# Performance work log

Measured on AMD Instinct MI355X. Metric: run time of the kernel, lower is better.

The kernel has to match this reference:

```python
import jax, jax.numpy as jnp
import numpy as np

D_MODEL = 512
N_HEADS = 8
D_K = D_MODEL // N_HEADS  # 64
MAX_LEN = 5000


def _positional_encoding(d_model, max_len):
    pe = np.zeros((max_len, d_model), dtype=np.float32)
    position = np.arange(max_len, dtype=np.float32)[:, None]
    div_term = np.exp(np.arange(0, d_model, 2, dtype=np.float32) * (-np.log(10000.0) / d_model))
    pe[:, 0::2] = np.sin(position * div_term)
    pe[:, 1::2] = np.cos(position * div_term)
    return jnp.asarray(pe)


def _layer_norm(x, gamma, beta, eps):
    mu = jnp.mean(x, axis=-1, keepdims=True)
    var = jnp.mean(jnp.square(x - mu), axis=-1, keepdims=True)
    return (x - mu) * jax.lax.rsqrt(var + eps) * gamma + beta


def setup_inputs() -> dict:
    key = jax.random.key(0)
    ks = jax.random.split(key, 5)
    s = 1.0 / np.sqrt(D_MODEL)
    return {
        "x": jax.random.normal(ks[0], (4, 2048, D_MODEL), dtype=jnp.float32),
        "ln1_g": jnp.ones((D_MODEL,), jnp.float32),
        "ln1_b": jnp.zeros((D_MODEL,), jnp.float32),
        "wq": jax.random.normal(ks[1], (D_MODEL, D_MODEL), jnp.float32) * s,
        "wk": jax.random.normal(ks[2], (D_MODEL, D_MODEL), jnp.float32) * s,
        "wv": jax.random.normal(ks[3], (D_MODEL, D_MODEL), jnp.float32) * s,
        "wfc": jax.random.normal(ks[4], (D_MODEL, D_MODEL), jnp.float32) * s,
        "ln2_g": jnp.ones((D_MODEL,), jnp.float32),
        "ln2_b": jnp.zeros((D_MODEL,), jnp.float32),
    }


def reference(x, ln1_g, ln1_b, wq, wk, wv, wfc, ln2_g, ln2_b):
    B, T, D = x.shape
    residual0 = x
    # outer pre-norm (nn.LayerNorm default eps=1e-5)
    h = _layer_norm(x, ln1_g, ln1_b, 1e-5)
    # sinusoidal positional encoding
    h = h + _positional_encoding(D_MODEL, MAX_LEN)[:T]
    residual1 = h
    # projections -> [B, H, T, d]
    q = (h @ wq).reshape(B, T, N_HEADS, D_K).transpose(0, 2, 1, 3)
    k = (h @ wk).reshape(B, T, N_HEADS, D_K).transpose(0, 2, 1, 3)
    v = (h @ wv).reshape(B, T, N_HEADS, D_K).transpose(0, 2, 1, 3)
    scale = 1.0 / np.sqrt(D_K).astype(np.float32)
    attn = jnp.einsum("bhqd,bhkd->bhqk", q * scale, k)
    causal = jnp.tril(jnp.ones((T, T), dtype=bool))  # subsequent mask
    attn = jnp.where(causal, attn, jnp.float32(-1e9))
    attn = jax.nn.softmax(attn, axis=-1)
    o = jnp.einsum("bhqk,bhkd->bhqd", attn, v)
    o = o.transpose(0, 2, 1, 3).reshape(B, T, D)
    o = o @ wfc
    # inner post-attention residual + LayerNorm (eps=1e-6)
    h2 = _layer_norm(o + residual1, ln2_g, ln2_b, 1e-6)
    return h2 + residual0
```

## Files before the change

kernel.cpp:

```cpp
#include <hip/hip_runtime.h>
#include <hip/hip_bf16.h>

#define B_ 4
#define T_ 2048
#define D_ 512

typedef __attribute__((ext_vector_type(8))) short short8;
typedef __attribute__((ext_vector_type(4))) short short4v;
typedef __attribute__((ext_vector_type(4))) float float4v;
typedef unsigned short bf16_t;

__device__ __forceinline__ bf16_t f2bf(float f) {
  unsigned int u = __builtin_bit_cast(unsigned int, f);
  unsigned int r = (u + 0x7fffu + ((u >> 16) & 1u)) >> 16;
  return (bf16_t)r;
}
__device__ __forceinline__ float bf2f(bf16_t b) {
  unsigned int u = ((unsigned int)b) << 16;
  return __builtin_bit_cast(float, u);
}

__device__ __forceinline__ float fast_exp2(float x) {
#if __has_builtin(__builtin_amdgcn_exp2f)
  return __builtin_amdgcn_exp2f(x);
#else
  float r;
  asm("v_exp_f32 %0, %1" : "=v"(r) : "v"(x));
  return r;
#endif
}

__device__ __forceinline__ unsigned cvt_pk_bf16(float lo, float hi) {
  unsigned r;
  asm("v_cvt_pk_bf16_f32 %0, %1, %2" : "=v"(r) : "v"(lo), "v"(hi));
  return r;
}

__device__ __forceinline__ float waveReduceSum(float v) {
#pragma unroll
  for (int m = 32; m >= 1; m >>= 1) v += __shfl_xor(v, m, 64);
  return v;
}

__device__ __forceinline__ void gld16(const bf16_t* g, bf16_t* l) {
  __builtin_amdgcn_global_load_lds(
      (const __attribute__((address_space(1))) void*)g,
      (__attribute__((address_space(3))) void*)l, 16, 0, 0);
}

__global__ __launch_bounds__(256) void pre_kernel(
    const float* __restrict__ x, const float* __restrict__ g,
    const float* __restrict__ bb,
    const float* __restrict__ wq, const float* __restrict__ wk,
    const float* __restrict__ wv, const float* __restrict__ wfc,
    bf16_t* __restrict__ h_bf16,
    bf16_t* __restrict__ wqkvT, bf16_t* __restrict__ wfcT) {
  if (blockIdx.x >= 2048) {
    int bid = blockIdx.x - 2048;
#pragma unroll 4
    for (int i = 0; i < 16; ++i) {
      int idx = bid * 4096 + i * 256 + threadIdx.x;
      if (idx < 786432) {
        int n = idx >> 9, k = idx & 511;
        const float* src = (n < 512) ? wq : ((n < 1024) ? wk : wv);
        float scl = (n < 512) ? 1.4426950408889634f
                              : ((n < 1024) ? 0.125f : 1.0f);
        int c = n & 511;
        wqkvT[idx] = f2bf(src[k * 512 + c] * scl);
      } else {
        int j = idx - 786432;
        int n = j >> 9, k = j & 511;
        wfcT[j] = f2bf(wfc[k * 512 + n]);
      }
    }
    return;
  }
  int wave = threadIdx.x >> 6, lane = threadIdx.x & 63;
  int row = blockIdx.x * 4 + wave;
  int pos = row & (T_ - 1);
  const float* xr = x + (size_t)row * D_;
  int c0 = lane * 8;
  float v[8];
  float4 a = *(const float4*)(xr + c0);
  float4 b4 = *(const float4*)(xr + c0 + 4);
  v[0]=a.x; v[1]=a.y; v[2]=a.z; v[3]=a.w;
  v[4]=b4.x; v[5]=b4.y; v[6]=b4.z; v[7]=b4.w;
  float s = 0.f;
#pragma unroll
  for (int j = 0; j < 8; ++j) s += v[j];
  s = waveReduceSum(s);
  float mu = s * (1.f / 512.f);
  float q = 0.f;
#pragma unroll
  for (int j = 0; j < 8; ++j) { float d = v[j] - mu; q += d * d; }
  q = waveReduceSum(q);
  float rstd = rsqrtf(q * (1.f / 512.f) + 1e-5f);
  bf16_t* hb = h_bf16 + (size_t)row * D_;
  float fpos = (float)pos;
#pragma unroll
  for (int jp = 0; jp < 4; ++jp) {
    int col = c0 + jp * 2;
    float dt = fast_exp2((float)col * (-13.287712379549449f / 512.0f));
    float ang = fpos * dt;
    float hn0 = (v[2 * jp] - mu) * rstd * g[col] + bb[col] + __sinf(ang);
    float hn1 = (v[2 * jp + 1] - mu) * rstd * g[col + 1] + bb[col + 1] + __cosf(ang);
    hb[col] = f2bf(hn0);
    hb[col + 1] = f2bf(hn1);
  }
}

template <typename EPI>
__device__ __forceinline__ void gemm_body(const bf16_t* __restrict__ A,
                                          const bf16_t* __restrict__ Bt,
                                          int m0, int n0, bf16_t* As, bf16_t* Bs,
                                          EPI epi) {
  const int tid = threadIdx.x;
  const int w = tid >> 6, lane = tid & 63;
  const int ln = lane & 15, quad = lane >> 4;
  const int wy = w >> 1, wx = w & 1;
  const int sw = ln & 7;

  float4v acc[4][4];
  float4v z = {0.f, 0.f, 0.f, 0.f};
#pragma unroll
  for (int i = 0; i < 4; ++i)
#pragma unroll
    for (int j = 0; j < 4; ++j) acc[i][j] = z;

  for (int k0 = 0; k0 < 512; k0 += 64) {
#pragma unroll
    for (int i = 0; i < 4; ++i) {
      int cbase = w * 256 + i * 64;
      int chunk = cbase + lane;
      int row = chunk >> 3;
      int lb = (chunk & 7) ^ (row & 7);
      gld16(A + (size_t)(m0 + row) * 512 + k0 + lb * 8, As + cbase * 8);
      gld16(Bt + (size_t)(n0 + row) * 512 + k0 + lb * 8, Bs + cbase * 8);
    }
    __syncthreads();
#pragma unroll
    for (int c = 0; c < 2; ++c) {
      short8 af[4], bf[4];
#pragma unroll
      for (int mt = 0; mt < 4; ++mt)
        af[mt] = *(const short8*)(As + (wy * 64 + mt * 16 + ln) * 64 + (((c * 4 + quad) ^ sw)) * 8);
#pragma unroll
      for (int nt = 0; nt < 4; ++nt)
        bf[nt] = *(const short8*)(Bs + (wx * 64 + nt * 16 + ln) * 64 + (((c * 4 + quad) ^ sw)) * 8);
#pragma unroll
      for (int mt = 0; mt < 4; ++mt)
#pragma unroll
        for (int nt = 0; nt < 4; ++nt)
          acc[mt][nt] = __builtin_amdgcn_mfma_f32_16x16x32_bf16(af[mt], bf[nt], acc[mt][nt], 0, 0, 0);
    }
    __syncthreads();
  }
#pragma unroll
  for (int mt = 0; mt < 4; ++mt)
#pragma unroll
    for (int r = 0; r < 4; ++r) {
      int row = m0 + wy * 64 + mt * 16 + quad * 4 + r;
#pragma unroll
      for (int nt = 0; nt < 4; ++nt) {
        int col = n0 + wx * 64 + nt * 16 + ln;
        epi(row, col, acc[mt][nt][r]);
      }
    }
}

__global__ __launch_bounds__(256) void gemm_qkvt_kernel(
    const bf16_t* __restrict__ h_bf, const bf16_t* __restrict__ wqkvT,
    bf16_t* __restrict__ qk, bf16_t* __restrict__ vT) {
  __shared__ __align__(16) bf16_t As[128 * 64];
  __shared__ __align__(16) bf16_t Bs[128 * 64];
  int bx = blockIdx.x;
  if (bx < 512) {
    int m0 = (bx >> 3) * 128, n0 = (bx & 7) * 128;
    gemm_body(h_bf, wqkvT, m0, n0, As, Bs,
              [&](int row, int col, float v) { qk[(size_t)row * 1024 + col] = f2bf(v); });
  } else {
    int local = bx - 512;
    int m0 = (local >> 6) * 128, n0 = (local & 63) * 128;
    gemm_body(wqkvT + 1024 * 512, h_bf, m0, n0, As, Bs,
              [&](int row, int col, float v) { vT[(size_t)row * 8192 + col] = f2bf(v); });
  }
}

__global__ __launch_bounds__(256) void gemm_out_kernel(
    const bf16_t* __restrict__ attn, const bf16_t* __restrict__ wfcT,
    const bf16_t* __restrict__ h_bf, bf16_t* __restrict__ o2r) {
  __shared__ __align__(16) bf16_t As[128 * 64];
  __shared__ __align__(16) bf16_t Bs[128 * 64];
  int bx = blockIdx.x;
  int m0 = (bx >> 2) * 128, n0 = (bx & 3) * 128;
  gemm_body(attn, wfcT, m0, n0, As, Bs, [&](int row, int col, float v) {
    size_t o = (size_t)row * 512 + col;
    o2r[o] = f2bf(v + bf2f(h_bf[o]));
  });
}

__global__ __launch_bounds__(256) void attn_kernel(const bf16_t* __restrict__ qk,
                                                   const bf16_t* __restrict__ vT,
                                                   bf16_t* __restrict__ out) {
  __shared__ __align__(16) bf16_t Ks[2][64 * 64];
  __shared__ __align__(16) bf16_t Vs[2][64 * 64];
  const int bx = blockIdx.x;
  const int qt = 31 - (bx >> 5);
  const int bh = bx & 31;
  const int b = bh >> 3, h = bh & 7;
  const int tid = threadIdx.x;
  const int w = tid >> 6, lane = tid & 63;
  const int ln = lane & 15, quad = lane >> 4;
  const int sw = ln & 7;

  short8 qf0, qf1;
  {
    size_t qrow = ((size_t)b * T_ + qt * 64 + w * 16 + ln) * 1024 + h * 64;
    qf0 = *(const short8*)(qk + qrow + quad * 8);
    qf1 = *(const short8*)(qk + qrow + 32 + quad * 8);
  }
  float4v z = {0.f, 0.f, 0.f, 0.f};
  float4v oacc[4];
#pragma unroll
  for (int i = 0; i < 4; ++i) oacc[i] = z;
  float m_s = -1e30f, l_s = 0.f;

  const bf16_t* kbase = qk + (size_t)b * T_ * 1024 + 512 + h * 64;
  const bf16_t* vbase = vT + (size_t)(h * 64) * 8192 + (size_t)b * T_;

  const int cb0 = w * 128, cb1 = w * 128 + 64;
  const int ch0 = cb0 + lane, ch1 = cb1 + lane;
  const int r0 = ch0 >> 3, r1 = ch1 >> 3;
  const int lb0 = (ch0 & 7) ^ (r0 & 7), lb1 = (ch1 & 7) ^ (r1 & 7);
  const bf16_t* kg0 = kbase + (size_t)r0 * 1024 + lb0 * 8;
  const bf16_t* kg1 = kbase + (size_t)r1 * 1024 + lb1 * 8;
  const bf16_t* vg0 = vbase + (size_t)r0 * 8192 + lb0 * 8;
  const bf16_t* vg1 = vbase + (size_t)r1 * 8192 + lb1 * 8;

  auto stage2 = [&](int buf) {
    gld16(kg0, Ks[buf] + cb0 * 8);
    gld16(kg1, Ks[buf] + cb1 * 8);
    gld16(vg0, Vs[buf] + cb0 * 8);
    gld16(vg1, Vs[buf] + cb1 * 8);
    kg0 += 64 * 1024; kg1 += 64 * 1024;
    vg0 += 64;        vg1 += 64;
  };

  auto compute = [&](const bf16_t* Kc, const bf16_t* Vc, bool mask) {
    float sv[4][4];
#pragma unroll
    for (int mt = 0; mt < 4; ++mt) {
      float4v st = z;
      int row = mt * 16 + ln;
      short8 a0 = *(const short8*)(Kc + row * 64 + ((0 + quad) ^ sw) * 8);
      short8 a1 = *(const short8*)(Kc + row * 64 + ((4 + quad) ^ sw) * 8);
      st = __builtin_amdgcn_mfma_f32_16x16x32_bf16(a0, qf0, st, 0, 0, 0);
      st = __builtin_amdgcn_mfma_f32_16x16x32_bf16(a1, qf1, st, 0, 0, 0);
#pragma unroll
      for (int r = 0; r < 4; ++r) {
        float v = st[r];
        if (mask) {
          int kloc = mt * 16 + quad * 4 + r;
          if (kloc > w * 16 + ln) v = -1e30f;
        }
        sv[mt][r] = v;
      }
    }
    float mx = sv[0][0];
#pragma unroll
    for (int mt = 0; mt < 4; ++mt)
#pragma unroll
      for (int r = 0; r < 4; ++r) mx = fmaxf(mx, sv[mt][r]);
    mx = fmaxf(mx, __shfl_xor(mx, 16, 64));
    mx = fmaxf(mx, __shfl_xor(mx, 32, 64));
    if (!__all(mx <= m_s + 8.0f)) {
      float mn = fmaxf(m_s, mx);
      float alpha = fast_exp2(m_s - mn);
      m_s = mn;
      l_s *= alpha;
#pragma unroll
      for (int dt = 0; dt < 4; ++dt)
#pragma unroll
        for (int r = 0; r < 4; ++r) oacc[dt][r] *= alpha;
    }
    float rs = 0.f;
#pragma unroll
    for (int mt = 0; mt < 4; ++mt)
#pragma unroll
      for (int r = 0; r < 4; ++r) {
        float p = fast_exp2(sv[mt][r] - m_s);
        sv[mt][r] = p;
        rs += p;
      }
    rs += __shfl_xor(rs, 16, 64);
    rs += __shfl_xor(rs, 32, 64);
    l_s += rs;
    short4v pf[4];
#pragma unroll
    for (int mt = 0; mt < 4; ++mt) {
      uint2 pp;
      pp.x = cvt_pk_bf16(sv[mt][0], sv[mt][1]);
      pp.y = cvt_pk_bf16(sv[mt][2], sv[mt][3]);
      pf[mt] = __builtin_bit_cast(short4v, pp);
    }
#pragma unroll
    for (int dt = 0; dt < 4; ++dt) {
      int row = dt * 16 + ln;
#pragma unroll
      for (int mt = 0; mt < 4; ++mt) {
        short4v av = *(const short4v*)(Vc + row * 64 + ((2 * mt + (quad >> 1)) ^ sw) * 8 + (quad & 1) * 4);
        oacc[dt] = __builtin_amdgcn_mfma_f32_16x16x16bf16_1k(av, pf[mt], oacc[dt], 0, 0, 0);
      }
    }
  };

  stage2(0);
  __syncthreads();
  for (int kt = 0; kt < qt; ++kt) {
    int cur = kt & 1;
    stage2(cur ^ 1);
    compute(Ks[cur], Vs[cur], false);
    __syncthreads();
  }
  compute(Ks[qt & 1], Vs[qt & 1], true);

  float inv = 1.0f / l_s;
  size_t obase = ((size_t)b * T_ + qt * 64 + w * 16 + ln) * 512 + h * 64;
#pragma unroll
  for (int dt = 0; dt < 4; ++dt) {
    short4v o4;
#pragma unroll
    for (int r = 0; r < 4; ++r) o4[r] = (short)f2bf(oacc[dt][r] * inv);
    *(short4v*)(out + obase + dt * 16 + quad * 4) = o4;
  }
}

__global__ __launch_bounds__(256) void ln2_kernel(
    const bf16_t* __restrict__ o2r, const float* __restrict__ x,
    const float* __restrict__ g, const float* __restrict__ bb,
    float* __restrict__ out) {
  int wave = threadIdx.x >> 6, lane = threadIdx.x & 63;
  int row = blockIdx.x * 4 + wave;
  size_t ro = (size_t)row * D_;
  int c0 = lane * 8;
  short8 ov = *(const short8*)(o2r + ro + c0);
  float t[8];
#pragma unroll
  for (int j = 0; j < 8; ++j) t[j] = bf2f((bf16_t)ov[j]);
  float s = 0.f;
#pragma unroll
  for (int j = 0; j < 8; ++j) s += t[j];
  s = waveReduceSum(s);
  float mu = s * (1.f / 512.f);
  float q = 0.f;
#pragma unroll
  for (int j = 0; j < 8; ++j) { float d = t[j] - mu; q += d * d; }
  q = waveReduceSum(q);
  float rstd = rsqrtf(q * (1.f / 512.f) + 1e-6f);
  float4 x0 = *(const float4*)(x + ro + c0);
  float4 x1 = *(const float4*)(x + ro + c0 + 4);
  float xr[8] = {x0.x, x0.y, x0.z, x0.w, x1.x, x1.y, x1.z, x1.w};
  float o[8];
#pragma unroll
  for (int j = 0; j < 8; ++j) {
    int col = c0 + j;
    o[j] = (t[j] - mu) * rstd * g[col] + bb[col] + xr[j];
  }
  float4 w0 = {o[0], o[1], o[2], o[3]};
  float4 w1 = {o[4], o[5], o[6], o[7]};
  *(float4*)(out + ro + c0) = w0;
  *(float4*)(out + ro + c0 + 4) = w1;
}

extern "C" void kernel_launch(void* const* d_in, const int* in_sizes, int n_in,
                              void* d_out, int out_size, void* d_ws, size_t ws_size,
                              hipStream_t stream) {
  const float* x   = (const float*)d_in[0];
  const float* g1  = (const float*)d_in[1];
  const float* b1  = (const float*)d_in[2];
  const float* wq  = (const float*)d_in[3];
  const float* wk  = (const float*)d_in[4];
  const float* wv  = (const float*)d_in[5];
  const float* wfc = (const float*)d_in[6];
  const float* g2  = (const float*)d_in[7];
  const float* b2  = (const float*)d_in[8];
  float* out = (float*)d_out;

  char* ws = (char*)d_ws;
  const size_t O_HBF  = 0;
  const size_t O_WQKV = 8388608;
  const size_t O_WFC  = 9961472;
  const size_t O_QK   = 10485760;
  const size_t O_VT   = 27262976;
  const size_t O_ATTN = 35651584;
  const size_t O_O2R  = 44040192;
  const size_t WS_NEED = 52428800;
  if (ws_size < WS_NEED) return;

  bf16_t* h_bf  = (bf16_t*)(ws + O_HBF);
  bf16_t* wqkvT = (bf16_t*)(ws + O_WQKV);
  bf16_t* wfcT  = (bf16_t*)(ws + O_WFC);
  bf16_t* qk    = (bf16_t*)(ws + O_QK);
  bf16_t* vT    = (bf16_t*)(ws + O_VT);
  bf16_t* attn  = (bf16_t*)(ws + O_ATTN);
  bf16_t* o2r   = (bf16_t*)(ws + O_O2R);

  pre_kernel<<<dim3(2304), dim3(256), 0, stream>>>(x, g1, b1, wq, wk, wv, wfc,
                                                   h_bf, wqkvT, wfcT);
  gemm_qkvt_kernel<<<dim3(768), dim3(256), 0, stream>>>(h_bf, wqkvT, qk, vT);
  attn_kernel<<<dim3(1024), dim3(256), 0, stream>>>(qk, vT, attn);
  gemm_out_kernel<<<dim3(256), dim3(256), 0, stream>>>(attn, wfcT, h_bf, o2r);
  ln2_kernel<<<dim3(2048), dim3(256), 0, stream>>>(o2r, x, g2, b2, out);
}
```

Measured before the change: 180.7 us.

## Split causal attention KV range across two blocks and merge with combine kernel

Each query tile's key range is split into two halves handled by separate blocks, doubling the attention grid. Each half writes an unnormalized partial output plus its per-row max and sum. A new combine kernel rescales and merges the two partials into the final attention output. This aims to improve load balance and occupancy across the causal triangle, at the cost of an extra kernel launch and additional memory traffic for the partials and stats. The max and sum reductions were also reshaped into shallower trees.

```diff
diff --git a/kernel.cpp b/kernel.cpp
--- a/kernel.cpp
+++ b/kernel.cpp
@@ -201,18 +201,26 @@
 
 __global__ __launch_bounds__(256) void attn_kernel(const bf16_t* __restrict__ qk,
                                                    const bf16_t* __restrict__ vT,
-                                                   bf16_t* __restrict__ out) {
+                                                   bf16_t* __restrict__ p0,
+                                                   bf16_t* __restrict__ p1,
+                                                   float2* __restrict__ stats) {
   __shared__ __align__(16) bf16_t Ks[2][64 * 64];
   __shared__ __align__(16) bf16_t Vs[2][64 * 64];
   const int bx = blockIdx.x;
-  const int qt = 31 - (bx >> 5);
-  const int bh = bx & 31;
+  const int qt = 31 - (bx >> 6);
+  const int rest = bx & 63;
+  const int half = rest & 1;
+  const int bh = rest >> 1;
   const int b = bh >> 3, h = bh & 7;
   const int tid = threadIdx.x;
   const int w = tid >> 6, lane = tid & 63;
   const int ln = lane & 15, quad = lane >> 4;
   const int sw = ln & 7;
 
+  const int nlo = (qt + 2) >> 1;
+  const int kt0 = half ? nlo : 0;
+  const int ktN = half ? (qt + 1) : nlo;
+
   short8 qf0, qf1;
   {
     size_t qrow = ((size_t)b * T_ + qt * 64 + w * 16 + ln) * 1024 + h * 64;
@@ -232,10 +240,10 @@
   const int ch0 = cb0 + lane, ch1 = cb1 + lane;
   const int r0 = ch0 >> 3, r1 = ch1 >> 3;
   const int lb0 = (ch0 & 7) ^ (r0 & 7), lb1 = (ch1 & 7) ^ (r1 & 7);
-  const bf16_t* kg0 = kbase + (size_t)r0 * 1024 + lb0 * 8;
-  const bf16_t* kg1 = kbase + (size_t)r1 * 1024 + lb1 * 8;
-  const bf16_t* vg0 = vbase + (size_t)r0 * 8192 + lb0 * 8;
-  const bf16_t* vg1 = vbase + (size_t)r1 * 8192 + lb1 * 8;
+  const bf16_t* kg0 = kbase + (size_t)(kt0 * 64 + r0) * 1024 + lb0 * 8;
+  const bf16_t* kg1 = kbase + (size_t)(kt0 * 64 + r1) * 1024 + lb1 * 8;
+  const bf16_t* vg0 = vbase + (size_t)r0 * 8192 + kt0 * 64 + lb0 * 8;
+  const bf16_t* vg1 = vbase + (size_t)r1 * 8192 + kt0 * 64 + lb1 * 8;
 
   auto stage2 = [&](int buf) {
     gld16(kg0, Ks[buf] + cb0 * 8);
@@ -266,11 +274,11 @@
         sv[mt][r] = v;
       }
     }
-    float mx = sv[0][0];
+    float mxa[4];
 #pragma unroll
     for (int mt = 0; mt < 4; ++mt)
-#pragma unroll
-      for (int r = 0; r < 4; ++r) mx = fmaxf(mx, sv[mt][r]);
+      mxa[mt] = fmaxf(fmaxf(sv[mt][0], sv[mt][1]), fmaxf(sv[mt][2], sv[mt][3]));
+    float mx = fmaxf(fmaxf(mxa[0], mxa[1]), fmaxf(mxa[2], mxa[3]));
     mx = fmaxf(mx, __shfl_xor(mx, 16, 64));
     mx = fmaxf(mx, __shfl_xor(mx, 32, 64));
     if (!__all(mx <= m_s + 8.0f)) {
@@ -283,15 +291,14 @@
 #pragma unroll
         for (int r = 0; r < 4; ++r) oacc[dt][r] *= alpha;
     }
-    float rs = 0.f;
-#pragma unroll
-    for (int mt = 0; mt < 4; ++mt)
-#pragma unroll
-      for (int r = 0; r < 4; ++r) {
-        float p = fast_exp2(sv[mt][r] - m_s);
-        sv[mt][r] = p;
-        rs += p;
-      }
+    float rsa[4];
+#pragma unroll
+    for (int mt = 0; mt < 4; ++mt) {
+#pragma unroll
+      for (int r = 0; r < 4; ++r) sv[mt][r] = fast_exp2(sv[mt][r] - m_s);
+      rsa[mt] = (sv[mt][0] + sv[mt][1]) + (sv[mt][2] + sv[mt][3]);
+    }
+    float rs = (rsa[0] + rsa[1]) + (rsa[2] + rsa[3]);
     rs += __shfl_xor(rs, 16, 64);
     rs += __shfl_xor(rs, 32, 64);
     l_s += rs;
@@ -314,25 +321,55 @@
     }
   };
 
-  stage2(0);
-  __syncthreads();
-  for (int kt = 0; kt < qt; ++kt) {
-    int cur = kt & 1;
-    stage2(cur ^ 1);
-    compute(Ks[cur], Vs[cur], false);
+  if (ktN > kt0) {
+    const int nt = ktN - kt0;
+    stage2(0);
     __syncthreads();
-  }
-  compute(Ks[qt & 1], Vs[qt & 1], true);
-
-  float inv = 1.0f / l_s;
+    for (int i = 0; i < nt - 1; ++i) {
+      int cur = i & 1;
+      stage2(cur ^ 1);
+      compute(Ks[cur], Vs[cur], false);
+      __syncthreads();
+    }
+    compute(Ks[(nt - 1) & 1], Vs[(nt - 1) & 1], (ktN - 1) == qt);
+  }
+
+  bf16_t* dst = half ? p1 : p0;
   size_t obase = ((size_t)b * T_ + qt * 64 + w * 16 + ln) * 512 + h * 64;
 #pragma unroll
   for (int dt = 0; dt < 4; ++dt) {
     short4v o4;
 #pragma unroll
-    for (int r = 0; r < 4; ++r) o4[r] = (short)f2bf(oacc[dt][r] * inv);
-    *(short4v*)(out + obase + dt * 16 + quad * 4) = o4;
-  }
+    for (int r = 0; r < 4; ++r) o4[r] = (short)f2bf(oacc[dt][r]);
+    *(short4v*)(dst + obase + dt * 16 + quad * 4) = o4;
+  }
+  if (quad == 0) {
+    int grow = b * T_ + qt * 64 + w * 16 + ln;
+    float2 st; st.x = m_s; st.y = l_s;
+    stats[half * 65536 + grow * 8 + h] = st;
+  }
+}
+
+__global__ __launch_bounds__(256) void combine_kernel(
+    bf16_t* __restrict__ p0, const bf16_t* __restrict__ p1,
+    const float2* __restrict__ stats) {
+  int wave = threadIdx.x >> 6, lane = threadIdx.x & 63;
+  int row = blockIdx.x * 4 + wave;
+  int h = lane >> 3;
+  float2 s0 = stats[row * 8 + h];
+  float2 s1 = stats[65536 + row * 8 + h];
+  float m = fmaxf(s0.x, s1.x);
+  float w0 = fast_exp2(s0.x - m), w1 = fast_exp2(s1.x - m);
+  float inv = 1.0f / (s0.y * w0 + s1.y * w1);
+  float a0 = w0 * inv, a1 = w1 * inv;
+  size_t ro = (size_t)row * 512 + lane * 8;
+  short8 l8 = *(const short8*)(p0 + ro);
+  short8 h8 = *(const short8*)(p1 + ro);
+  short8 o8;
+#pragma unroll
+  for (int j = 0; j < 8; ++j)
+    o8[j] = (short)f2bf(bf2f((bf16_t)l8[j]) * a0 + bf2f((bf16_t)h8[j]) * a1);
+  *(short8*)(p0 + ro) = o8;
 }
 
 __global__ __launch_bounds__(256) void ln2_kernel(
@@ -404,11 +441,13 @@
   bf16_t* vT    = (bf16_t*)(ws + O_VT);
   bf16_t* attn  = (bf16_t*)(ws + O_ATTN);
   bf16_t* o2r   = (bf16_t*)(ws + O_O2R);
+  float2* stats = (float2*)(ws + O_WQKV);
 
   pre_kernel<<<dim3(2304), dim3(256), 0, stream>>>(x, g1, b1, wq, wk, wv, wfc,
                                                    h_bf, wqkvT, wfcT);
   gemm_qkvt_kernel<<<dim3(768), dim3(256), 0, stream>>>(h_bf, wqkvT, qk, vT);
-  attn_kernel<<<dim3(1024), dim3(256), 0, stream>>>(qk, vT, attn);
+  attn_kernel<<<dim3(2048), dim3(256), 0, stream>>>(qk, vT, attn, o2r, stats);
+  combine_kernel<<<dim3(2048), dim3(256), 0, stream>>>(attn, o2r, stats);
   gemm_out_kernel<<<dim3(256), dim3(256), 0, stream>>>(attn, wfcT, h_bf, o2r);
   ln2_kernel<<<dim3(2048), dim3(256), 0, stream>>>(o2r, x, g2, b2, out);
 }
```

After: 183.4 us. About the same (+1.5%).
